# Kernel optimization log

Hardware: AMD Instinct MI355X
Metric: run time of the kernel (lower is better)

Reference implementation:

```python
import jax, jax.numpy as jnp
import numpy as np

GAMMA = 0.99
LAM = 0.95
EPS = 1e-8


def setup_inputs() -> dict:
    key = jax.random.key(0)
    k1, k2, k3 = jax.random.split(key, 3)
    T, N = 2048, 8192
    rewards = jax.random.normal(k1, (T, N), dtype=jnp.float32)
    values = jax.random.normal(k2, (T + 1, N), dtype=jnp.float32)
    dones = jax.random.randint(k3, (T, N), 0, 2, dtype=jnp.int32)
    return {"rewards": rewards, "values": values, "dones": dones}


def reference(rewards, values, dones):
    # rewards: [T, N], values: [T+1, N], dones: [T, N]
    nonterminal = 1.0 - dones.astype(rewards.dtype)        # [T, N]
    # delta_t = r_t + gamma * V_{t+1} * nt_t - V_t
    delta = rewards + GAMMA * values[1:] * nonterminal - values[:-1]
    coef = (GAMMA * LAM) * nonterminal                      # [T, N]

    def step(carry, xs):
        d, c = xs
        a = d + c * carry
        return a, a

    init = jnp.zeros(rewards.shape[1], dtype=rewards.dtype)
    _, advantages = jax.lax.scan(step, init, (delta, coef), reverse=True)
    returns = advantages + values[:-1]
    # torch .std() is unbiased (ddof=1)
    mean = advantages.mean()
    std = advantages.std(ddof=1)
    advantages_norm = (advantages - mean) / (std + EPS)
    return advantages_norm, returns
```

## Files before the change

kernel.cpp:

```cpp
#include <hip/hip_runtime.h>
#include <math.h>

#define GAMMA_ 0.99f
#define GL_ (0.99f * 0.95f)
#define L_ 32

__global__ __launch_bounds__(256)
void gae_pass1(const float4* __restrict__ rw, const float4* __restrict__ vv,
               const int4* __restrict__ dn,
               float4* __restrict__ A, float4* __restrict__ B,
               float4* __restrict__ Sa, float4* __restrict__ Sa2,
               float4* __restrict__ SaP, float4* __restrict__ SP,
               float4* __restrict__ SP2, uint4* __restrict__ mask,
               int T, int N4)
{
    int q = blockIdx.x * blockDim.x + threadIdx.x;
    int chunk = blockIdx.y;
    if (q >= N4) return;
    int s = chunk * L_;
    int e = s + L_; if (e > T) e = T;

    float a[4] = {0.f,0.f,0.f,0.f}, P[4] = {1.f,1.f,1.f,1.f};
    float sa[4] = {0.f,0.f,0.f,0.f}, sa2[4] = {0.f,0.f,0.f,0.f};
    float saP[4] = {0.f,0.f,0.f,0.f}, sP[4] = {0.f,0.f,0.f,0.f};
    float sP2[4] = {0.f,0.f,0.f,0.f};
    unsigned mm[4] = {0u,0u,0u,0u};

    float4 vn4 = vv[(size_t)e * N4 + q];
    float vnext[4] = {vn4.x, vn4.y, vn4.z, vn4.w};

    #pragma unroll 2
    for (int t = e - 1; t >= s; --t) {
        size_t off = (size_t)t * N4 + q;
        float4 r4 = rw[off];
        int4   d4 = dn[off];
        float4 v4 = vv[off];
        float rr[4] = {r4.x, r4.y, r4.z, r4.w};
        int   dd[4] = {d4.x, d4.y, d4.z, d4.w};
        float vc[4] = {v4.x, v4.y, v4.z, v4.w};
        unsigned bit = 1u << (t - s);
        #pragma unroll
        for (int j = 0; j < 4; ++j) {
            float nt = (dd[j] == 0) ? 1.0f : 0.0f;
            float delta = rr[j] + GAMMA_ * vnext[j] * nt - vc[j];
            float c = GL_ * nt;
            a[j] = delta + c * a[j];
            P[j] = c * P[j];
            sa[j]  += a[j];
            sa2[j] += a[j] * a[j];
            saP[j] += a[j] * P[j];
            sP[j]  += P[j];
            sP2[j] += P[j] * P[j];
            if (dd[j] == 0) mm[j] |= bit;
            vnext[j] = vc[j];
        }
    }
    size_t idx = (size_t)chunk * N4 + q;
    A[idx]   = make_float4(a[0], a[1], a[2], a[3]);
    B[idx]   = make_float4(P[0], P[1], P[2], P[3]);
    Sa[idx]  = make_float4(sa[0], sa[1], sa[2], sa[3]);
    Sa2[idx] = make_float4(sa2[0], sa2[1], sa2[2], sa2[3]);
    SaP[idx] = make_float4(saP[0], saP[1], saP[2], saP[3]);
    SP[idx]  = make_float4(sP[0], sP[1], sP[2], sP[3]);
    SP2[idx] = make_float4(sP2[0], sP2[1], sP2[2], sP2[3]);
    mask[idx] = make_uint4(mm[0], mm[1], mm[2], mm[3]);
}

__global__ __launch_bounds__(64)
void gae_pass2(const float* __restrict__ A, const float* __restrict__ B,
               const float* __restrict__ Sa, const float* __restrict__ Sa2,
               const float* __restrict__ SaP, const float* __restrict__ SP,
               const float* __restrict__ SP2,
               float* __restrict__ carry, double* __restrict__ sums,
               int N, int C)
{
    int n = blockIdx.x * blockDim.x + threadIdx.x;
    double lsum = 0.0, lsq = 0.0;
    if (n < N) {
        float g = 0.f;
        for (int i = C - 1; i >= 0; --i) {
            int idx = i * N + n;
            carry[idx] = g;
            float e = g;
            lsum += (double)(Sa[idx] + SP[idx] * e);
            lsq  += (double)(Sa2[idx] + 2.0f * e * SaP[idx] + (e * e) * SP2[idx]);
            g = A[idx] + B[idx] * g;
        }
    }
    for (int off = 32; off > 0; off >>= 1) {
        lsum += __shfl_down(lsum, off, 64);
        lsq  += __shfl_down(lsq, off, 64);
    }
    if ((threadIdx.x & 63) == 0) {
        atomicAdd(&sums[0], lsum);
        atomicAdd(&sums[1], lsq);
    }
}

__global__ __launch_bounds__(256)
void gae_pass3(const float4* __restrict__ rw, const float4* __restrict__ vv,
               const uint4* __restrict__ mask, const float4* __restrict__ carry,
               const double* __restrict__ sums,
               float4* __restrict__ out_adv, float4* __restrict__ out_ret,
               int T, int N4, double Minv, double Mm1inv)
{
    int q = blockIdx.x * blockDim.x + threadIdx.x;
    int chunk = blockIdx.y;
    if (q >= N4) return;
    int s = chunk * L_;
    int e = s + L_; if (e > T) e = T;

    double S = sums[0], S2 = sums[1];
    float mean = (float)(S * Minv);
    double vard = (S2 - S * S * Minv) * Mm1inv;
    float inv = (float)(1.0 / (sqrt(vard) + 1e-8));

    size_t idx = (size_t)chunk * N4 + q;
    float4 c4 = carry[idx];
    uint4  m4 = mask[idx];
    float a[4] = {c4.x, c4.y, c4.z, c4.w};
    unsigned mm[4] = {m4.x, m4.y, m4.z, m4.w};

    float4 vn4 = vv[(size_t)e * N4 + q];
    float vnext[4] = {vn4.x, vn4.y, vn4.z, vn4.w};

    #pragma unroll 2
    for (int t = e - 1; t >= s; --t) {
        size_t off = (size_t)t * N4 + q;
        float4 r4 = rw[off];
        float4 v4 = vv[off];
        float rr[4] = {r4.x, r4.y, r4.z, r4.w};
        float vc[4] = {v4.x, v4.y, v4.z, v4.w};
        float oa[4], orr[4];
        unsigned bit = 1u << (t - s);
        #pragma unroll
        for (int j = 0; j < 4; ++j) {
            float nt = (mm[j] & bit) ? 1.0f : 0.0f;
            float delta = rr[j] + GAMMA_ * vnext[j] * nt - vc[j];
            a[j] = delta + GL_ * nt * a[j];
            oa[j]  = (a[j] - mean) * inv;
            orr[j] = a[j] + vc[j];
            vnext[j] = vc[j];
        }
        out_adv[off] = make_float4(oa[0], oa[1], oa[2], oa[3]);
        out_ret[off] = make_float4(orr[0], orr[1], orr[2], orr[3]);
    }
}

extern "C" void kernel_launch(void* const* d_in, const int* in_sizes, int n_in,
                              void* d_out, int out_size, void* d_ws, size_t ws_size,
                              hipStream_t stream)
{
    const float* rw = (const float*)d_in[0];
    const float* vv = (const float*)d_in[1];
    const int*   dn = (const int*)d_in[2];

    long long TN = in_sizes[0];
    long long VN = in_sizes[1];
    int N = (int)(VN - TN);
    int T = (int)(TN / N);
    int N4 = N / 4;
    int C = (T + L_ - 1) / L_;

    char* ws = (char*)d_ws;
    double* sums = (double*)ws;
    size_t cn = (size_t)C * N;
    unsigned* mask = (unsigned*)(ws + 16);
    float* f   = (float*)(ws + 16 + cn * 4);
    float* A   = f;
    float* B   = f + cn;
    float* Sa  = f + 2 * cn;
    float* Sa2 = f + 3 * cn;
    float* SaP = f + 4 * cn;
    float* SP  = f + 5 * cn;
    float* SP2 = f + 6 * cn;
    float* cry = f + 7 * cn;

    hipMemsetAsync(d_ws, 0, 16, stream);

    dim3 blk(256);
    dim3 g1((N4 + 255) / 256, C);
    gae_pass1<<<g1, blk, 0, stream>>>(
        (const float4*)rw, (const float4*)vv, (const int4*)dn,
        (float4*)A, (float4*)B, (float4*)Sa, (float4*)Sa2, (float4*)SaP,
        (float4*)SP, (float4*)SP2, (uint4*)mask, T, N4);

    gae_pass2<<<dim3((N + 63) / 64), dim3(64), 0, stream>>>(
        A, B, Sa, Sa2, SaP, SP, SP2, cry, sums, N, C);

    double M = (double)TN;
    gae_pass3<<<g1, blk, 0, stream>>>(
        (const float4*)rw, (const float4*)vv, (const uint4*)mask,
        (const float4*)cry, sums,
        (float4*)d_out, (float4*)((float*)d_out + TN),
        T, N4, 1.0 / M, 1.0 / (M - 1.0));
}
```

Measured before the change: 333.6 us.

## Narrow vector width to float2, parallel-scan pass2 across chunks, nontemporal IO

Passes 1 and 3 switch from float4 to float2 per thread, doubling the thread count, and raise the unroll factor to 4. Pass 2 replaces the per-column sequential loop over chunks with a wave-level parallel scan, one wave per column, each lane handling one chunk, used when there are at most 64 chunks. Reductions go through shared memory with one atomic per block, and nontemporal loads and stores are used for dones and the outputs. This aims to shorten the serial pass 2 and improve latency hiding. The cost is strided, poorly coalesced loads in pass 2 (lanes read across chunks, stride N) and narrower memory transactions in passes 1 and 3.

```diff
diff --git a/kernel.cpp b/kernel.cpp
--- a/kernel.cpp
+++ b/kernel.cpp
@@ -5,44 +5,44 @@
 #define GL_ (0.99f * 0.95f)
 #define L_ 32
 
+typedef float    f2 __attribute__((ext_vector_type(2)));
+typedef int      i2 __attribute__((ext_vector_type(2)));
+typedef unsigned u2 __attribute__((ext_vector_type(2)));
+
 __global__ __launch_bounds__(256)
-void gae_pass1(const float4* __restrict__ rw, const float4* __restrict__ vv,
-               const int4* __restrict__ dn,
-               float4* __restrict__ A, float4* __restrict__ B,
-               float4* __restrict__ Sa, float4* __restrict__ Sa2,
-               float4* __restrict__ SaP, float4* __restrict__ SP,
-               float4* __restrict__ SP2, uint4* __restrict__ mask,
-               int T, int N4)
+void gae_pass1(const f2* __restrict__ rw, const f2* __restrict__ vv,
+               const i2* __restrict__ dn,
+               f2* __restrict__ A, f2* __restrict__ B,
+               f2* __restrict__ Sa, f2* __restrict__ Sa2,
+               f2* __restrict__ SaP, f2* __restrict__ SP,
+               f2* __restrict__ SP2, u2* __restrict__ mask,
+               int T, int N2)
 {
     int q = blockIdx.x * blockDim.x + threadIdx.x;
     int chunk = blockIdx.y;
-    if (q >= N4) return;
+    if (q >= N2) return;
     int s = chunk * L_;
     int e = s + L_; if (e > T) e = T;
 
-    float a[4] = {0.f,0.f,0.f,0.f}, P[4] = {1.f,1.f,1.f,1.f};
-    float sa[4] = {0.f,0.f,0.f,0.f}, sa2[4] = {0.f,0.f,0.f,0.f};
-    float saP[4] = {0.f,0.f,0.f,0.f}, sP[4] = {0.f,0.f,0.f,0.f};
-    float sP2[4] = {0.f,0.f,0.f,0.f};
-    unsigned mm[4] = {0u,0u,0u,0u};
-
-    float4 vn4 = vv[(size_t)e * N4 + q];
-    float vnext[4] = {vn4.x, vn4.y, vn4.z, vn4.w};
-
-    #pragma unroll 2
+    float a[2]  = {0.f,0.f}, P[2]   = {1.f,1.f};
+    float sa[2] = {0.f,0.f}, sa2[2] = {0.f,0.f};
+    float saP[2]= {0.f,0.f}, sP[2]  = {0.f,0.f}, sP2[2] = {0.f,0.f};
+    unsigned mm[2] = {0u,0u};
+
+    f2 vn = vv[(size_t)e * N2 + q];
+    float vnext[2] = {vn.x, vn.y};
+
+    #pragma unroll 4
     for (int t = e - 1; t >= s; --t) {
-        size_t off = (size_t)t * N4 + q;
-        float4 r4 = rw[off];
-        int4   d4 = dn[off];
-        float4 v4 = vv[off];
-        float rr[4] = {r4.x, r4.y, r4.z, r4.w};
-        int   dd[4] = {d4.x, d4.y, d4.z, d4.w};
-        float vc[4] = {v4.x, v4.y, v4.z, v4.w};
+        size_t off = (size_t)t * N2 + q;
+        f2 r2 = rw[off];
+        i2 d2 = __builtin_nontemporal_load(&dn[off]);
+        f2 v2 = vv[off];
         unsigned bit = 1u << (t - s);
         #pragma unroll
-        for (int j = 0; j < 4; ++j) {
-            float nt = (dd[j] == 0) ? 1.0f : 0.0f;
-            float delta = rr[j] + GAMMA_ * vnext[j] * nt - vc[j];
+        for (int j = 0; j < 2; ++j) {
+            float nt = (d2[j] == 0) ? 1.0f : 0.0f;
+            float delta = r2[j] + GAMMA_ * vnext[j] * nt - v2[j];
             float c = GL_ * nt;
             a[j] = delta + c * a[j];
             P[j] = c * P[j];
@@ -51,28 +51,83 @@
             saP[j] += a[j] * P[j];
             sP[j]  += P[j];
             sP2[j] += P[j] * P[j];
-            if (dd[j] == 0) mm[j] |= bit;
-            vnext[j] = vc[j];
+            mm[j] |= (d2[j] == 0) ? bit : 0u;
+            vnext[j] = v2[j];
         }
     }
-    size_t idx = (size_t)chunk * N4 + q;
-    A[idx]   = make_float4(a[0], a[1], a[2], a[3]);
-    B[idx]   = make_float4(P[0], P[1], P[2], P[3]);
-    Sa[idx]  = make_float4(sa[0], sa[1], sa[2], sa[3]);
-    Sa2[idx] = make_float4(sa2[0], sa2[1], sa2[2], sa2[3]);
-    SaP[idx] = make_float4(saP[0], saP[1], saP[2], saP[3]);
-    SP[idx]  = make_float4(sP[0], sP[1], sP[2], sP[3]);
-    SP2[idx] = make_float4(sP2[0], sP2[1], sP2[2], sP2[3]);
-    mask[idx] = make_uint4(mm[0], mm[1], mm[2], mm[3]);
+    size_t idx = (size_t)chunk * N2 + q;
+    f2 o;
+    o.x = a[0];   o.y = a[1];   A[idx]   = o;
+    o.x = P[0];   o.y = P[1];   B[idx]   = o;
+    o.x = sa[0];  o.y = sa[1];  Sa[idx]  = o;
+    o.x = sa2[0]; o.y = sa2[1]; Sa2[idx] = o;
+    o.x = saP[0]; o.y = saP[1]; SaP[idx] = o;
+    o.x = sP[0];  o.y = sP[1];  SP[idx]  = o;
+    o.x = sP2[0]; o.y = sP2[1]; SP2[idx] = o;
+    u2 om; om.x = mm[0]; om.y = mm[1];
+    mask[idx] = om;
+}
+
+__global__ __launch_bounds__(1024)
+void gae_pass2_ws(const float* __restrict__ A, const float* __restrict__ B,
+                  const float* __restrict__ Sa, const float* __restrict__ Sa2,
+                  const float* __restrict__ SaP, const float* __restrict__ SP,
+                  const float* __restrict__ SP2,
+                  float* __restrict__ carry, double* __restrict__ sums,
+                  int N, int C)
+{
+    __shared__ double psum[16], psq[16];
+    int wid  = threadIdx.x >> 6;
+    int lane = threadIdx.x & 63;
+    int nwav = blockDim.x >> 6;
+    int n = blockIdx.x * nwav + wid;
+
+    float Ah = 0.f, Bh = 1.f;
+    float sa = 0.f, sa2 = 0.f, saP = 0.f, sp = 0.f, sp2 = 0.f;
+    bool act = (n < N) && (lane < C);
+    size_t idx = (size_t)lane * N + n;
+    if (act) {
+        Ah = A[idx];  Bh = B[idx];
+        sa = Sa[idx]; sa2 = Sa2[idx]; saP = SaP[idx];
+        sp = SP[idx]; sp2 = SP2[idx];
+    }
+
+    #pragma unroll
+    for (int d = 1; d < 64; d <<= 1) {
+        float Ad = __shfl_down(Ah, d, 64);
+        float Bd = __shfl_down(Bh, d, 64);
+        if (lane + d < 64) { Ah = fmaf(Bh, Ad, Ah); Bh *= Bd; }
+    }
+    float e = __shfl_down(Ah, 1, 64);
+    if (lane == 63) e = 0.f;
+
+    double lsum = 0.0, lsq = 0.0;
+    if (act) {
+        carry[idx] = e;
+        lsum = (double)(sa + sp * e);
+        lsq  = (double)(sa2 + 2.0f * e * saP + (e * e) * sp2);
+    }
+    for (int off = 32; off > 0; off >>= 1) {
+        lsum += __shfl_down(lsum, off, 64);
+        lsq  += __shfl_down(lsq, off, 64);
+    }
+    if (lane == 0) { psum[wid] = lsum; psq[wid] = lsq; }
+    __syncthreads();
+    if (threadIdx.x == 0) {
+        double s = 0.0, s2 = 0.0;
+        for (int w = 0; w < nwav; ++w) { s += psum[w]; s2 += psq[w]; }
+        atomicAdd(&sums[0], s);
+        atomicAdd(&sums[1], s2);
+    }
 }
 
 __global__ __launch_bounds__(64)
-void gae_pass2(const float* __restrict__ A, const float* __restrict__ B,
-               const float* __restrict__ Sa, const float* __restrict__ Sa2,
-               const float* __restrict__ SaP, const float* __restrict__ SP,
-               const float* __restrict__ SP2,
-               float* __restrict__ carry, double* __restrict__ sums,
-               int N, int C)
+void gae_pass2_seq(const float* __restrict__ A, const float* __restrict__ B,
+                   const float* __restrict__ Sa, const float* __restrict__ Sa2,
+                   const float* __restrict__ SaP, const float* __restrict__ SP,
+                   const float* __restrict__ SP2,
+                   float* __restrict__ carry, double* __restrict__ sums,
+                   int N, int C)
 {
     int n = blockIdx.x * blockDim.x + threadIdx.x;
     double lsum = 0.0, lsq = 0.0;
@@ -98,15 +153,15 @@
 }
 
 __global__ __launch_bounds__(256)
-void gae_pass3(const float4* __restrict__ rw, const float4* __restrict__ vv,
-               const uint4* __restrict__ mask, const float4* __restrict__ carry,
+void gae_pass3(const f2* __restrict__ rw, const f2* __restrict__ vv,
+               const u2* __restrict__ mask, const f2* __restrict__ carry,
                const double* __restrict__ sums,
-               float4* __restrict__ out_adv, float4* __restrict__ out_ret,
-               int T, int N4, double Minv, double Mm1inv)
+               f2* __restrict__ out_adv, f2* __restrict__ out_ret,
+               int T, int N2, double Minv, double Mm1inv)
 {
     int q = blockIdx.x * blockDim.x + threadIdx.x;
     int chunk = blockIdx.y;
-    if (q >= N4) return;
+    if (q >= N2) return;
     int s = chunk * L_;
     int e = s + L_; if (e > T) e = T;
 
@@ -115,35 +170,33 @@
     double vard = (S2 - S * S * Minv) * Mm1inv;
     float inv = (float)(1.0 / (sqrt(vard) + 1e-8));
 
-    size_t idx = (size_t)chunk * N4 + q;
-    float4 c4 = carry[idx];
-    uint4  m4 = mask[idx];
-    float a[4] = {c4.x, c4.y, c4.z, c4.w};
-    unsigned mm[4] = {m4.x, m4.y, m4.z, m4.w};
-
-    float4 vn4 = vv[(size_t)e * N4 + q];
-    float vnext[4] = {vn4.x, vn4.y, vn4.z, vn4.w};
-
-    #pragma unroll 2
+    size_t idx = (size_t)chunk * N2 + q;
+    f2 c2 = carry[idx];
+    u2 m2 = mask[idx];
+    float a[2] = {c2.x, c2.y};
+    unsigned mm[2] = {m2.x, m2.y};
+
+    f2 vn = vv[(size_t)e * N2 + q];
+    float vnext[2] = {vn.x, vn.y};
+
+    #pragma unroll 4
     for (int t = e - 1; t >= s; --t) {
-        size_t off = (size_t)t * N4 + q;
-        float4 r4 = rw[off];
-        float4 v4 = vv[off];
-        float rr[4] = {r4.x, r4.y, r4.z, r4.w};
-        float vc[4] = {v4.x, v4.y, v4.z, v4.w};
-        float oa[4], orr[4];
+        size_t off = (size_t)t * N2 + q;
+        f2 r2 = rw[off];
+        f2 v2 = vv[off];
         unsigned bit = 1u << (t - s);
+        f2 oa, orr;
         #pragma unroll
-        for (int j = 0; j < 4; ++j) {
+        for (int j = 0; j < 2; ++j) {
             float nt = (mm[j] & bit) ? 1.0f : 0.0f;
-            float delta = rr[j] + GAMMA_ * vnext[j] * nt - vc[j];
+            float delta = r2[j] + GAMMA_ * vnext[j] * nt - v2[j];
             a[j] = delta + GL_ * nt * a[j];
             oa[j]  = (a[j] - mean) * inv;
-            orr[j] = a[j] + vc[j];
-            vnext[j] = vc[j];
+            orr[j] = a[j] + v2[j];
+            vnext[j] = v2[j];
         }
-        out_adv[off] = make_float4(oa[0], oa[1], oa[2], oa[3]);
-        out_ret[off] = make_float4(orr[0], orr[1], orr[2], orr[3]);
+        __builtin_nontemporal_store(oa,  &out_adv[off]);
+        __builtin_nontemporal_store(orr, &out_ret[off]);
     }
 }
 
@@ -159,7 +212,7 @@
     long long VN = in_sizes[1];
     int N = (int)(VN - TN);
     int T = (int)(TN / N);
-    int N4 = N / 4;
+    int N2 = N / 2;
     int C = (T + L_ - 1) / L_;
 
     char* ws = (char*)d_ws;
@@ -179,19 +232,25 @@
     hipMemsetAsync(d_ws, 0, 16, stream);
 
     dim3 blk(256);
-    dim3 g1((N4 + 255) / 256, C);
+    dim3 g1((N2 + 255) / 256, C);
     gae_pass1<<<g1, blk, 0, stream>>>(
-        (const float4*)rw, (const float4*)vv, (const int4*)dn,
-        (float4*)A, (float4*)B, (float4*)Sa, (float4*)Sa2, (float4*)SaP,
-        (float4*)SP, (float4*)SP2, (uint4*)mask, T, N4);
-
-    gae_pass2<<<dim3((N + 63) / 64), dim3(64), 0, stream>>>(
-        A, B, Sa, Sa2, SaP, SP, SP2, cry, sums, N, C);
+        (const f2*)rw, (const f2*)vv, (const i2*)dn,
+        (f2*)A, (f2*)B, (f2*)Sa, (f2*)Sa2, (f2*)SaP,
+        (f2*)SP, (f2*)SP2, (u2*)mask, T, N2);
+
+    if (C <= 64) {
+        int wpb = 16;
+        gae_pass2_ws<<<dim3((N + wpb - 1) / wpb), dim3(wpb * 64), 0, stream>>>(
+            A, B, Sa, Sa2, SaP, SP, SP2, cry, sums, N, C);
+    } else {
+        gae_pass2_seq<<<dim3((N + 63) / 64), dim3(64), 0, stream>>>(
+            A, B, Sa, Sa2, SaP, SP, SP2, cry, sums, N, C);
+    }
 
     double M = (double)TN;
     gae_pass3<<<g1, blk, 0, stream>>>(
-        (const float4*)rw, (const float4*)vv, (const uint4*)mask,
-        (const float4*)cry, sums,
-        (float4*)d_out, (float4*)((float*)d_out + TN),
-        T, N4, 1.0 / M, 1.0 / (M - 1.0));
-}
+        (const f2*)rw, (const f2*)vv, (const u2*)mask,
+        (const f2*)cry, sums,
+        (f2*)d_out, (f2*)((float*)d_out + TN),
+        T, N2, 1.0 / M, 1.0 / (M - 1.0));
+}
```

After: 318.4 us. -4.6%, faster.
